# Performance work log

Measured on AMD Instinct MI355X. Metric: run time of the kernel, lower is better.

The kernel has to match this reference:

```python
import jax, jax.numpy as jnp
import numpy as np

HIDDEN = 1024
HEADS = 16
HEAD_DIM = 64
EPS = 0.001  # numerical_stabilizer


def setup_inputs() -> dict:
    key = jax.random.key(0)
    kq, kk, kv, kwq, kwk, kwv = jax.random.split(key, 6)
    B, S = 4, 4096
    shape = (B, S, HIDDEN)
    # glorot_uniform over (hidden, heads*head_dim) fan
    init = jax.nn.initializers.glorot_uniform()
    wshape = (HIDDEN, HEADS, HEAD_DIM)
    return {
        "query": jax.random.normal(kq, shape, jnp.float32),
        "key": jax.random.normal(kk, shape, jnp.float32),
        "value": jax.random.normal(kv, shape, jnp.float32),
        "query_kernel": init(kwq, wshape, jnp.float32),
        "key_kernel": init(kwk, wshape, jnp.float32),
        "value_kernel": init(kwv, wshape, jnp.float32),
    }


def reference(query, key, value, query_kernel, key_kernel, value_kernel):
    # project: [b,s,d] x [d,n,h] -> [b,s,n,h]
    q = jnp.einsum('bsd,dnh->bsnh', query, query_kernel)
    k = jnp.einsum('bsd,dnh->bsnh', key, key_kernel)
    v = jnp.einsum('bsd,dnh->bsnh', value, value_kernel)
    # relu feature map + stabilizer
    q = jax.nn.relu(q) + EPS
    k = jax.nn.relu(k) + EPS
    # kv aggregation: [b,n,h_k,h_v]
    kvs = jnp.einsum('bsnm,bsnd->bnmd', k, v)
    a_v = jnp.einsum('bsnm,bnmd->bsnd', q, kvs)
    ks_sum = jnp.sum(k, axis=1)                 # [b,n,m]
    normalizer = jnp.einsum('bsnm,bnm->bsn', q, ks_sum)
    a_v = a_v / normalizer[..., None]
    B, S, N, H = a_v.shape
    return a_v.reshape(B, S, N * H)
```

## Files before the change

kernel.cpp:

```cpp
#include <hip/hip_runtime.h>
#include <hip/hip_bf16.h>
#include <cstdint>
#include <cstddef>

#define HIDDEN 1024
#define NHEADS 16
#define HD     64
#define BATCH  4
#define SEQ    4096
#define MTOT   (BATCH*SEQ)
#define EPSF   1e-3f

typedef unsigned short u16;
typedef unsigned int   u32;
typedef __bf16 bf16x8 __attribute__((ext_vector_type(8)));
typedef u16    u16x8  __attribute__((ext_vector_type(8)));
typedef float  f32x4  __attribute__((ext_vector_type(4)));
typedef u32    u32x4  __attribute__((ext_vector_type(4)));

__device__ inline u16 f2bf(float a) {
    __bf16 h = (__bf16)a;
    return __builtin_bit_cast(u16, h);
}
__device__ inline u32 pack2bf(float a, float b) {
    return (u32)f2bf(a) | ((u32)f2bf(b) << 16);
}
__device__ inline float bf2f(u16 x) {
    return __builtin_bit_cast(float, (u32)x << 16);
}
__device__ inline f32x4 mfma16(bf16x8 a, bf16x8 b, f32x4 c) {
    return __builtin_amdgcn_mfma_f32_16x16x32_bf16(a, b, c, 0, 0, 0);
}
__device__ inline void gl_lds16(const void* g, void* l) {
    __builtin_amdgcn_global_load_lds(
        (const __attribute__((address_space(1))) void*)g,
        (__attribute__((address_space(3))) void*)l,
        16, 0, 0);
}

__global__ __launch_bounds__(256) void prep_kernel(
    const float* __restrict__ W0, const float* __restrict__ W1,
    const float* __restrict__ W2, u16* __restrict__ Wt,
    float* __restrict__ zero_base)
{
    const int t = threadIdx.x;
    if (blockIdx.z == 3) {
        const int base = (blockIdx.y * 16 + blockIdx.x) * 256 + t;
        const int total = 64*64*64 + 64*64;
        for (int idx = base; idx < total; idx += 65536) zero_base[idx] = 0.f;
        return;
    }
    const int z = blockIdx.z;
    const float* __restrict__ W = (z == 0) ? W0 : ((z == 1) ? W1 : W2);
    u16* __restrict__ Wz = Wt + (size_t)z * HIDDEN * HIDDEN;
    const int d0 = blockIdx.y * 64, c0 = blockIdx.x * 64;
    __shared__ u16 T[64 * 72];
    {
        const int r = t & 63, p = t >> 6;
        const float* src = W + (size_t)(d0 + r) * HIDDEN + c0 + p * 16;
        f32x4 x0 = *(const f32x4*)src,       x1 = *(const f32x4*)(src + 4);
        f32x4 x2 = *(const f32x4*)(src + 8), x3 = *(const f32x4*)(src + 12);
        u32x4 y0 = { pack2bf(x0[0],x0[1]), pack2bf(x0[2],x0[3]),
                     pack2bf(x1[0],x1[1]), pack2bf(x1[2],x1[3]) };
        u32x4 y1 = { pack2bf(x2[0],x2[1]), pack2bf(x2[2],x2[3]),
                     pack2bf(x3[0],x3[1]), pack2bf(x3[2],x3[3]) };
        *(u32x4*)((char*)T + (size_t)(r * 72 + p * 16) * 2)     = y0;
        *(u32x4*)((char*)T + (size_t)(r * 72 + p * 16 + 8) * 2) = y1;
    }
    __syncthreads();
    {
        const int c = t & 63, p = t >> 6;
        u16 vals[16];
        #pragma unroll
        for (int i = 0; i < 16; ++i) vals[i] = T[(p * 16 + i) * 72 + c];
        u16* dst = Wz + (size_t)(c0 + c) * HIDDEN + d0 + p * 16;
        *(u16x8*)dst       = *(const u16x8*)&vals[0];
        *(u16x8*)(dst + 8) = *(const u16x8*)&vals[8];
    }
}

__global__ __launch_bounds__(256) void conv_kernel(
    const float* __restrict__ X0, const float* __restrict__ X1,
    const float* __restrict__ X2, u16* __restrict__ D0,
    u16* __restrict__ D1, u16* __restrict__ D2)
{
    const int z = blockIdx.y;
    const float* __restrict__ X = (z == 0) ? X0 : ((z == 1) ? X1 : X2);
    u16* __restrict__ D = (z == 0) ? D0 : ((z == 1) ? D1 : D2);
    const int ngrp = MTOT * HIDDEN / 8;
    for (int i = blockIdx.x * 256 + threadIdx.x; i < ngrp; i += 262144) {
        const size_t off = (size_t)i * 8;
        f32x4 a = *(const f32x4*)(X + off);
        f32x4 b = *(const f32x4*)(X + off + 4);
        u32x4 p = { pack2bf(a[0],a[1]), pack2bf(a[2],a[3]),
                    pack2bf(b[0],b[1]), pack2bf(b[2],b[3]) };
        *(u32x4*)(D + off) = p;
    }
}

__global__ __launch_bounds__(256) void gemm_proj(
    const u16* __restrict__ Xb, const u16* __restrict__ W,
    u16* __restrict__ Pz, const int doact)
{
    const int lin = blockIdx.y * 8 + blockIdx.x;
    const int swz = (lin & 7) * 128 + (lin >> 3);
    const int m0 = (swz >> 3) * 128;
    const int n0 = (swz & 7) * 128;

    __shared__ u16 As[128 * 64];
    __shared__ u16 Bs[128 * 64];

    const int t = threadIdx.x, lane = t & 63, wid = t >> 6;
    const int wr = (wid >> 1) * 64, wc = (wid & 1) * 64;
    const int l15 = lane & 15, l4 = lane >> 4;
    const int srow = lane >> 3;
    const int schunk = (lane & 7) ^ srow;

    f32x4 acc[4][4];
    #pragma unroll
    for (int i = 0; i < 4; ++i)
        #pragma unroll
        for (int j = 0; j < 4; ++j) acc[i][j] = f32x4{0.f, 0.f, 0.f, 0.f};

    for (int kt = 0; kt < HIDDEN / 64; ++kt) {
        const int k0 = kt * 64;
        __syncthreads();
        #pragma unroll
        for (int g = 0; g < 4; ++g) {
            const int rbase = wid * 32 + g * 8;
            const int r = rbase + srow;
            gl_lds16(Xb + (size_t)(m0 + r) * HIDDEN + k0 + schunk * 8,
                     &As[rbase * 64]);
            gl_lds16(W + (size_t)(n0 + r) * HIDDEN + k0 + schunk * 8,
                     &Bs[rbase * 64]);
        }
        __syncthreads();
        #pragma unroll
        for (int ks = 0; ks < 2; ++ks) {
            bf16x8 af[4], bfr[4];
            #pragma unroll
            for (int mi = 0; mi < 4; ++mi) {
                const int r = wr + mi * 16 + l15;
                const int c = (ks * 4 + l4) ^ (r & 7);
                af[mi] = *(const bf16x8*)((const char*)As + (size_t)r * 128 + c * 16);
            }
            #pragma unroll
            for (int ni = 0; ni < 4; ++ni) {
                const int r = wc + ni * 16 + l15;
                const int c = (ks * 4 + l4) ^ (r & 7);
                bfr[ni] = *(const bf16x8*)((const char*)Bs + (size_t)r * 128 + c * 16);
            }
            #pragma unroll
            for (int mi = 0; mi < 4; ++mi)
                #pragma unroll
                for (int ni = 0; ni < 4; ++ni)
                    acc[mi][ni] = mfma16(af[mi], bfr[ni], acc[mi][ni]);
        }
    }
    #pragma unroll
    for (int mi = 0; mi < 4; ++mi) {
        #pragma unroll
        for (int ni = 0; ni < 4; ++ni) {
            const int mrow = m0 + wr + mi * 16 + l4 * 4;
            const int ncol = n0 + wc + ni * 16 + l15;
            #pragma unroll
            for (int r = 0; r < 4; ++r) {
                float v = acc[mi][ni][r];
                if (doact) v = fmaxf(v, 0.f) + EPSF;
                Pz[(size_t)(mrow + r) * HIDDEN + ncol] = f2bf(v);
            }
        }
    }
}

__global__ __launch_bounds__(256) void kvs_kernel(
    const u16* __restrict__ Kp, const u16* __restrict__ Vp,
    float* __restrict__ kvsT, float* __restrict__ ks_sum)
{
    const int bn = blockIdx.x, sc = blockIdx.y;
    const int b = bn >> 4, n = bn & 15;
    __shared__ float Ks[64 * 64];
    __shared__ float Vs[64 * 64];
    const int t = threadIdx.x;
    const int tm = t & 15, td = t >> 4;
    float acc[4][4] = {};
    float ksa[4] = {0.f, 0.f, 0.f, 0.f};
    const size_t rowbase = ((size_t)b * SEQ + (size_t)sc * 256) * HIDDEN + n * 64;

    for (int st = 0; st < 4; ++st) {
        __syncthreads();
        #pragma unroll
        for (int i = 0; i < 2; ++i) {
            const int j = i * 256 + t;
            const int r = j >> 3, c = j & 7;
            const size_t off = rowbase + (size_t)(st * 64 + r) * HIDDEN + c * 8;
            u16x8 kk = *(const u16x8*)(Kp + off);
            u16x8 vv = *(const u16x8*)(Vp + off);
            f32x4 ka{bf2f(kk[0]), bf2f(kk[1]), bf2f(kk[2]), bf2f(kk[3])};
            f32x4 kb{bf2f(kk[4]), bf2f(kk[5]), bf2f(kk[6]), bf2f(kk[7])};
            f32x4 va{bf2f(vv[0]), bf2f(vv[1]), bf2f(vv[2]), bf2f(vv[3])};
            f32x4 vb{bf2f(vv[4]), bf2f(vv[5]), bf2f(vv[6]), bf2f(vv[7])};
            *(f32x4*)&Ks[r * 64 + c * 8]     = ka;
            *(f32x4*)&Ks[r * 64 + c * 8 + 4] = kb;
            *(f32x4*)&Vs[r * 64 + c * 8]     = va;
            *(f32x4*)&Vs[r * 64 + c * 8 + 4] = vb;
        }
        __syncthreads();
        for (int s = 0; s < 64; ++s) {
            const f32x4 kk = *(const f32x4*)&Ks[s * 64 + tm * 4];
            const f32x4 vv = *(const f32x4*)&Vs[s * 64 + td * 4];
            #pragma unroll
            for (int i = 0; i < 4; ++i) {
                ksa[i] += kk[i];
                #pragma unroll
                for (int j = 0; j < 4; ++j) acc[i][j] += kk[i] * vv[j];
            }
        }
    }
    float* kt_bn = kvsT + (size_t)bn * 64 * 64;
    #pragma unroll
    for (int j = 0; j < 4; ++j)
        #pragma unroll
        for (int i = 0; i < 4; ++i)
            atomicAdd(&kt_bn[(td * 4 + j) * 64 + tm * 4 + i], acc[i][j]);
    if (td == 0) {
        #pragma unroll
        for (int i = 0; i < 4; ++i)
            atomicAdd(&ks_sum[bn * 64 + tm * 4 + i], ksa[i]);
    }
}

__global__ __launch_bounds__(256) void out_kernel(
    const u16* __restrict__ Qp, const float* __restrict__ kvsT,
    const float* __restrict__ ks_sum, float* __restrict__ out)
{
    const int bn = blockIdx.x, sc = blockIdx.y;
    const int b = bn >> 4, n = bn & 15;
    __shared__ u16 Aq[256 * 64];
    __shared__ u16 Bk[64 * 64];
    __shared__ float ksl[64];
    __shared__ float nrm[256];
    const int t = threadIdx.x, lane = t & 63, wid = t >> 6;
    const int l15 = lane & 15, l4 = lane >> 4;
    const size_t qbase = ((size_t)b * SEQ + (size_t)sc * 256) * HIDDEN + n * 64;

    #pragma unroll
    for (int i = 0; i < 8; ++i) {
        const int j = i * 256 + t;
        const int r = j >> 3, c = j & 7;
        u16x8 q8 = *(const u16x8*)(Qp + qbase + (size_t)r * HIDDEN + c * 8);
        *(u16x8*)((char*)Aq + (size_t)r * 128 + ((c ^ (r & 7)) * 16)) = q8;
    }
    {
        const int d = t & 63, p = t >> 6;
        const float* src = kvsT + ((size_t)bn * 64 + d) * 64 + p * 16;
        f32x4 x0 = *(const f32x4*)src,        x1 = *(const f32x4*)(src + 4);
        f32x4 x2 = *(const f32x4*)(src + 8),  x3 = *(const f32x4*)(src + 12);
        u32x4 y0 = { pack2bf(x0[0],x0[1]), pack2bf(x0[2],x0[3]),
                     pack2bf(x1[0],x1[1]), pack2bf(x1[2],x1[3]) };
        u32x4 y1 = { pack2bf(x2[0],x2[1]), pack2bf(x2[2],x2[3]),
                     pack2bf(x3[0],x3[1]), pack2bf(x3[2],x3[3]) };
        *(u32x4*)((char*)Bk + (size_t)d * 128 + (((p * 2)     ^ (d & 7)) * 16)) = y0;
        *(u32x4*)((char*)Bk + (size_t)d * 128 + (((p * 2 + 1) ^ (d & 7)) * 16)) = y1;
    }
    if (t < 16) ((f32x4*)ksl)[t] = ((const f32x4*)(ks_sum + bn * 64))[t];
    __syncthreads();
    {
        float s = 0.f;
        #pragma unroll
        for (int c = 0; c < 8; ++c) {
            u16x8 q8 = *(const u16x8*)((const char*)Aq + (size_t)t * 128 + ((c ^ (t & 7)) * 16));
            #pragma unroll
            for (int e = 0; e < 8; ++e) s += bf2f(q8[e]) * ksl[c * 8 + e];
        }
        nrm[t] = s;
    }
    __syncthreads();
    f32x4 acc[4][4];
    #pragma unroll
    for (int i = 0; i < 4; ++i)
        #pragma unroll
        for (int j = 0; j < 4; ++j) acc[i][j] = f32x4{0.f, 0.f, 0.f, 0.f};
    #pragma unroll
    for (int ks = 0; ks < 2; ++ks) {
        bf16x8 af[4], bfr[4];
        #pragma unroll
        for (int mi = 0; mi < 4; ++mi) {
            const int r = wid * 64 + mi * 16 + l15;
            const int c = (ks * 4 + l4) ^ (r & 7);
            af[mi] = *(const bf16x8*)((const char*)Aq + (size_t)r * 128 + c * 16);
        }
        #pragma unroll
        for (int ni = 0; ni < 4; ++ni) {
            const int rd = ni * 16 + l15;
            const int c = (ks * 4 + l4) ^ (rd & 7);
            bfr[ni] = *(const bf16x8*)((const char*)Bk + (size_t)rd * 128 + c * 16);
        }
        #pragma unroll
        for (int mi = 0; mi < 4; ++mi)
            #pragma unroll
            for (int ni = 0; ni < 4; ++ni)
                acc[mi][ni] = mfma16(af[mi], bfr[ni], acc[mi][ni]);
    }
    const size_t obase = (size_t)b * SEQ + (size_t)sc * 256;
    #pragma unroll
    for (int mi = 0; mi < 4; ++mi) {
        const int s0l = wid * 64 + mi * 16 + l4 * 4;
        const float rn0 = 1.f / nrm[s0l],     rn1 = 1.f / nrm[s0l + 1];
        const float rn2 = 1.f / nrm[s0l + 2], rn3 = 1.f / nrm[s0l + 3];
        #pragma unroll
        for (int ni = 0; ni < 4; ++ni) {
            const int d = ni * 16 + l15;
            float* op = out + (obase + s0l) * (size_t)HIDDEN + n * 64 + d;
            op[0 * HIDDEN] = acc[mi][ni][0] * rn0;
            op[1 * HIDDEN] = acc[mi][ni][1] * rn1;
            op[2 * HIDDEN] = acc[mi][ni][2] * rn2;
            op[3 * HIDDEN] = acc[mi][ni][3] * rn3;
        }
    }
}

extern "C" void kernel_launch(void* const* d_in, const int* in_sizes, int n_in,
                              void* d_out, int out_size, void* d_ws, size_t ws_size,
                              hipStream_t stream)
{
    const float* Xq = (const float*)d_in[0];
    const float* Xk = (const float*)d_in[1];
    const float* Xv = (const float*)d_in[2];
    const float* Wq = (const float*)d_in[3];
    const float* Wk = (const float*)d_in[4];
    const float* Wv = (const float*)d_in[5];
    float* out = (float*)d_out;

    char* w = (char*)d_ws;
    u16*   Wt    = (u16*)w;
    u16*   slotA = (u16*)(w + 6291456);
    u16*   slotB = (u16*)(w + 6291456 + 1 * 33554432);
    u16*   slotC = (u16*)(w + 6291456 + 2 * 33554432);
    u16*   slotD = (u16*)(w + 6291456 + 3 * 33554432);
    float* kvsT  = (float*)(w + 6291456 + 4 * 33554432);
    float* ks    = (float*)(w + 6291456 + 4 * 33554432 + 1048576);

    prep_kernel<<<dim3(16, 16, 4), 256, 0, stream>>>(Wq, Wk, Wv, Wt, kvsT);
    conv_kernel<<<dim3(1024, 3), 256, 0, stream>>>(Xq, Xk, Xv, slotA, slotB, slotC);
    gemm_proj<<<dim3(8, 128), 256, 0, stream>>>(slotA, Wt,                 slotD, 1);
    gemm_proj<<<dim3(8, 128), 256, 0, stream>>>(slotB, Wt + 1048576,       slotA, 1);
    gemm_proj<<<dim3(8, 128), 256, 0, stream>>>(slotC, Wt + 2 * 1048576,   slotB, 0);
    kvs_kernel<<<dim3(64, 16), 256, 0, stream>>>(slotA, slotB, kvsT, ks);
    out_kernel<<<dim3(64, 16), 256, 0, stream>>>(slotD, kvsT, ks, out);
}
```

Baseline: 476.2 us.

## Fuse fp32-to-bf16 input conversion into projection GEMM and batch three projections

Removes the separate conversion kernel. The projection GEMM now reads fp32 activations directly, prefetching the next k-tile into registers and packing to bf16 into swizzled LDS. The three projection GEMMs are merged into one launch over blockIdx.z. This avoids writing and re-reading a bf16 copy of the 3x64MB inputs and drops two kernel launches. In exchange each tile reads twice the bytes, the A operand goes through registers instead of async global-to-LDS loads, and register pressure rises.

Result: faster. 465.2 us (-2.3%).

```diff
diff --git a/kernel.cpp b/kernel.cpp
--- a/kernel.cpp
+++ b/kernel.cpp
@@ -79,29 +79,17 @@
     }
 }
 
-__global__ __launch_bounds__(256) void conv_kernel(
+__global__ __launch_bounds__(256) void gemm_proj(
     const float* __restrict__ X0, const float* __restrict__ X1,
-    const float* __restrict__ X2, u16* __restrict__ D0,
-    u16* __restrict__ D1, u16* __restrict__ D2)
-{
-    const int z = blockIdx.y;
+    const float* __restrict__ X2, const u16* __restrict__ Wt,
+    u16* __restrict__ P)
+{
+    const int z = blockIdx.z;
     const float* __restrict__ X = (z == 0) ? X0 : ((z == 1) ? X1 : X2);
-    u16* __restrict__ D = (z == 0) ? D0 : ((z == 1) ? D1 : D2);
-    const int ngrp = MTOT * HIDDEN / 8;
-    for (int i = blockIdx.x * 256 + threadIdx.x; i < ngrp; i += 262144) {
-        const size_t off = (size_t)i * 8;
-        f32x4 a = *(const f32x4*)(X + off);
-        f32x4 b = *(const f32x4*)(X + off + 4);
-        u32x4 p = { pack2bf(a[0],a[1]), pack2bf(a[2],a[3]),
-                    pack2bf(b[0],b[1]), pack2bf(b[2],b[3]) };
-        *(u32x4*)(D + off) = p;
-    }
-}
-
-__global__ __launch_bounds__(256) void gemm_proj(
-    const u16* __restrict__ Xb, const u16* __restrict__ W,
-    u16* __restrict__ Pz, const int doact)
-{
+    const u16* __restrict__ W = Wt + (size_t)z * HIDDEN * HIDDEN;
+    u16* __restrict__ Pz = P + (size_t)z * ((size_t)MTOT * HIDDEN);
+    const int doact = (z < 2);
+
     const int lin = blockIdx.y * 8 + blockIdx.x;
     const int swz = (lin & 7) * 128 + (lin >> 3);
     const int m0 = (swz >> 3) * 128;
@@ -113,26 +101,49 @@
     const int t = threadIdx.x, lane = t & 63, wid = t >> 6;
     const int wr = (wid >> 1) * 64, wc = (wid & 1) * 64;
     const int l15 = lane & 15, l4 = lane >> 4;
-    const int srow = lane >> 3;
-    const int schunk = (lane & 7) ^ srow;
+    const int arow = t >> 3, acol = t & 7;
+    const int brow = lane >> 3;
+    const int bchunk = (lane & 7) ^ brow;
 
     f32x4 acc[4][4];
     #pragma unroll
     for (int i = 0; i < 4; ++i)
         #pragma unroll
         for (int j = 0; j < 4; ++j) acc[i][j] = f32x4{0.f, 0.f, 0.f, 0.f};
+
+    f32x4 a0[4], a1[4];
+    #pragma unroll
+    for (int i = 0; i < 4; ++i) {
+        const float* ap = X + (size_t)(m0 + arow + 32 * i) * HIDDEN + acol * 8;
+        a0[i] = *(const f32x4*)ap;
+        a1[i] = *(const f32x4*)(ap + 4);
+    }
 
     for (int kt = 0; kt < HIDDEN / 64; ++kt) {
         const int k0 = kt * 64;
         __syncthreads();
         #pragma unroll
+        for (int i = 0; i < 4; ++i) {
+            const int r = arow + 32 * i;
+            const int cd = acol ^ (r & 7);
+            u32x4 apk = { pack2bf(a0[i][0], a0[i][1]), pack2bf(a0[i][2], a0[i][3]),
+                          pack2bf(a1[i][0], a1[i][1]), pack2bf(a1[i][2], a1[i][3]) };
+            *(u32x4*)((char*)As + (size_t)r * 128 + cd * 16) = apk;
+        }
+        #pragma unroll
         for (int g = 0; g < 4; ++g) {
             const int rbase = wid * 32 + g * 8;
-            const int r = rbase + srow;
-            gl_lds16(Xb + (size_t)(m0 + r) * HIDDEN + k0 + schunk * 8,
-                     &As[rbase * 64]);
-            gl_lds16(W + (size_t)(n0 + r) * HIDDEN + k0 + schunk * 8,
+            gl_lds16(W + (size_t)(n0 + rbase + brow) * HIDDEN + k0 + bchunk * 8,
                      &Bs[rbase * 64]);
+        }
+        if (kt + 1 < HIDDEN / 64) {
+            #pragma unroll
+            for (int i = 0; i < 4; ++i) {
+                const float* ap = X + (size_t)(m0 + arow + 32 * i) * HIDDEN
+                                    + (k0 + 64) + acol * 8;
+                a0[i] = *(const f32x4*)ap;
+                a1[i] = *(const f32x4*)(ap + 4);
+            }
         }
         __syncthreads();
         #pragma unroll
@@ -333,19 +344,16 @@
     float* out = (float*)d_out;
 
     char* w = (char*)d_ws;
-    u16*   Wt    = (u16*)w;
-    u16*   slotA = (u16*)(w + 6291456);
-    u16*   slotB = (u16*)(w + 6291456 + 1 * 33554432);
-    u16*   slotC = (u16*)(w + 6291456 + 2 * 33554432);
-    u16*   slotD = (u16*)(w + 6291456 + 3 * 33554432);
-    float* kvsT  = (float*)(w + 6291456 + 4 * 33554432);
-    float* ks    = (float*)(w + 6291456 + 4 * 33554432 + 1048576);
+    u16*   Wt   = (u16*)w;
+    u16*   P    = (u16*)(w + 6291456);
+    u16*   Pq   = P;
+    u16*   Pk   = P + (size_t)MTOT * HIDDEN;
+    u16*   Pv   = P + 2 * (size_t)MTOT * HIDDEN;
+    float* kvsT = (float*)(w + 6291456 + 3 * 33554432);
+    float* ks   = (float*)(w + 6291456 + 3 * 33554432 + 1048576);
 
     prep_kernel<<<dim3(16, 16, 4), 256, 0, stream>>>(Wq, Wk, Wv, Wt, kvsT);
-    conv_kernel<<<dim3(1024, 3), 256, 0, stream>>>(Xq, Xk, Xv, slotA, slotB, slotC);
-    gemm_proj<<<dim3(8, 128), 256, 0, stream>>>(slotA, Wt,                 slotD, 1);
-    gemm_proj<<<dim3(8, 128), 256, 0, stream>>>(slotB, Wt + 1048576,       slotA, 1);
-    gemm_proj<<<dim3(8, 128), 256, 0, stream>>>(slotC, Wt + 2 * 1048576,   slotB, 0);
-    kvs_kernel<<<dim3(64, 16), 256, 0, stream>>>(slotA, slotB, kvsT, ks);
-    out_kernel<<<dim3(64, 16), 256, 0, stream>>>(slotD, kvsT, ks, out);
-}
+    gemm_proj<<<dim3(8, 128, 3), 256, 0, stream>>>(Xq, Xk, Xv, Wt, P);
+    kvs_kernel<<<dim3(64, 16), 256, 0, stream>>>(Pk, Pv, kvsT, ks);
+    out_kernel<<<dim3(64, 16), 256, 0, stream>>>(Pq, kvsT, ks, out);
+}
```

## Double-buffer GEMM LDS tiles, widen conv loads, halve kvs grid

Applied to the files above, without the earlier changes.

The projection GEMM now uses two LDS buffers, so the async global-to-LDS load of the next K tile is issued while MFMAs run on the current one, with one barrier per iteration instead of two. The conversion kernel is unrolled to a fixed four iterations of 16 elements per thread, giving more memory requests in flight. The kvs kernel processes 512 sequence rows per block over half as many blocks. Costs are doubled LDS use in the GEMM, which may reduce occupancy, and less parallelism in kvs.

Result: faster. 463.0 us (-2.8%).

```diff
diff --git a/kernel.cpp b/kernel.cpp
--- a/kernel.cpp
+++ b/kernel.cpp
@@ -87,14 +87,20 @@
     const int z = blockIdx.y;
     const float* __restrict__ X = (z == 0) ? X0 : ((z == 1) ? X1 : X2);
     u16* __restrict__ D = (z == 0) ? D0 : ((z == 1) ? D1 : D2);
-    const int ngrp = MTOT * HIDDEN / 8;
-    for (int i = blockIdx.x * 256 + threadIdx.x; i < ngrp; i += 262144) {
-        const size_t off = (size_t)i * 8;
-        f32x4 a = *(const f32x4*)(X + off);
-        f32x4 b = *(const f32x4*)(X + off + 4);
-        u32x4 p = { pack2bf(a[0],a[1]), pack2bf(a[2],a[3]),
-                    pack2bf(b[0],b[1]), pack2bf(b[2],b[3]) };
-        *(u32x4*)(D + off) = p;
+    const int tid = blockIdx.x * 256 + threadIdx.x;
+    #pragma unroll
+    for (int it = 0; it < 4; ++it) {
+        const size_t off = ((size_t)(it * 262144 + tid)) * 16;
+        f32x4 x0 = *(const f32x4*)(X + off);
+        f32x4 x1 = *(const f32x4*)(X + off + 4);
+        f32x4 x2 = *(const f32x4*)(X + off + 8);
+        f32x4 x3 = *(const f32x4*)(X + off + 12);
+        u32x4 p0 = { pack2bf(x0[0],x0[1]), pack2bf(x0[2],x0[3]),
+                     pack2bf(x1[0],x1[1]), pack2bf(x1[2],x1[3]) };
+        u32x4 p1 = { pack2bf(x2[0],x2[1]), pack2bf(x2[2],x2[3]),
+                     pack2bf(x3[0],x3[1]), pack2bf(x3[2],x3[3]) };
+        *(u32x4*)(D + off)     = p0;
+        *(u32x4*)(D + off + 8) = p1;
     }
 }
 
@@ -107,14 +113,14 @@
     const int m0 = (swz >> 3) * 128;
     const int n0 = (swz & 7) * 128;
 
-    __shared__ u16 As[128 * 64];
-    __shared__ u16 Bs[128 * 64];
+    __shared__ u16 As[2][128 * 64];
+    __shared__ u16 Bs[2][128 * 64];
 
     const int t = threadIdx.x, lane = t & 63, wid = t >> 6;
     const int wr = (wid >> 1) * 64, wc = (wid & 1) * 64;
     const int l15 = lane & 15, l4 = lane >> 4;
-    const int srow = lane >> 3;
-    const int schunk = (lane & 7) ^ srow;
+    const int brow = lane >> 3;
+    const int bchunk = (lane & 7) ^ brow;
 
     f32x4 acc[4][4];
     #pragma unroll
@@ -122,19 +128,26 @@
         #pragma unroll
         for (int j = 0; j < 4; ++j) acc[i][j] = f32x4{0.f, 0.f, 0.f, 0.f};
 
-    for (int kt = 0; kt < HIDDEN / 64; ++kt) {
-        const int k0 = kt * 64;
-        __syncthreads();
-        #pragma unroll
-        for (int g = 0; g < 4; ++g) {
-            const int rbase = wid * 32 + g * 8;
-            const int r = rbase + srow;
-            gl_lds16(Xb + (size_t)(m0 + r) * HIDDEN + k0 + schunk * 8,
-                     &As[rbase * 64]);
-            gl_lds16(W + (size_t)(n0 + r) * HIDDEN + k0 + schunk * 8,
-                     &Bs[rbase * 64]);
-        }
-        __syncthreads();
+#define STAGE(BUF, KT)                                                       \
+    {                                                                        \
+        _Pragma("unroll")                                                    \
+        for (int g = 0; g < 4; ++g) {                                        \
+            const int rbase = wid * 32 + g * 8;                              \
+            gl_lds16(Xb + (size_t)(m0 + rbase + brow) * HIDDEN               \
+                        + (KT) * 64 + bchunk * 8,                            \
+                     &As[BUF][rbase * 64]);                                  \
+            gl_lds16(W + (size_t)(n0 + rbase + brow) * HIDDEN                \
+                       + (KT) * 64 + bchunk * 8,                             \
+                     &Bs[BUF][rbase * 64]);                                  \
+        }                                                                    \
+    }
+
+    STAGE(0, 0);
+    __syncthreads();
+
+    for (int kt = 0; kt < 16; ++kt) {
+        const int cur = kt & 1;
+        if (kt + 1 < 16) STAGE(cur ^ 1, kt + 1);
         #pragma unroll
         for (int ks = 0; ks < 2; ++ks) {
             bf16x8 af[4], bfr[4];
@@ -142,13 +155,13 @@
             for (int mi = 0; mi < 4; ++mi) {
                 const int r = wr + mi * 16 + l15;
                 const int c = (ks * 4 + l4) ^ (r & 7);
-                af[mi] = *(const bf16x8*)((const char*)As + (size_t)r * 128 + c * 16);
+                af[mi] = *(const bf16x8*)((const char*)As[cur] + (size_t)r * 128 + c * 16);
             }
             #pragma unroll
             for (int ni = 0; ni < 4; ++ni) {
                 const int r = wc + ni * 16 + l15;
                 const int c = (ks * 4 + l4) ^ (r & 7);
-                bfr[ni] = *(const bf16x8*)((const char*)Bs + (size_t)r * 128 + c * 16);
+                bfr[ni] = *(const bf16x8*)((const char*)Bs[cur] + (size_t)r * 128 + c * 16);
             }
             #pragma unroll
             for (int mi = 0; mi < 4; ++mi)
@@ -156,7 +169,10 @@
                 for (int ni = 0; ni < 4; ++ni)
                     acc[mi][ni] = mfma16(af[mi], bfr[ni], acc[mi][ni]);
         }
-    }
+        __syncthreads();
+    }
+#undef STAGE
+
     #pragma unroll
     for (int mi = 0; mi < 4; ++mi) {
         #pragma unroll
@@ -185,9 +201,9 @@
     const int tm = t & 15, td = t >> 4;
     float acc[4][4] = {};
     float ksa[4] = {0.f, 0.f, 0.f, 0.f};
-    const size_t rowbase = ((size_t)b * SEQ + (size_t)sc * 256) * HIDDEN + n * 64;
-
-    for (int st = 0; st < 4; ++st) {
+    const size_t rowbase = ((size_t)b * SEQ + (size_t)sc * 512) * HIDDEN + n * 64;
+
+    for (int st = 0; st < 8; ++st) {
         __syncthreads();
         #pragma unroll
         for (int i = 0; i < 2; ++i) {
@@ -343,9 +359,9 @@
 
     prep_kernel<<<dim3(16, 16, 4), 256, 0, stream>>>(Wq, Wk, Wv, Wt, kvsT);
     conv_kernel<<<dim3(1024, 3), 256, 0, stream>>>(Xq, Xk, Xv, slotA, slotB, slotC);
-    gemm_proj<<<dim3(8, 128), 256, 0, stream>>>(slotA, Wt,                 slotD, 1);
-    gemm_proj<<<dim3(8, 128), 256, 0, stream>>>(slotB, Wt + 1048576,       slotA, 1);
-    gemm_proj<<<dim3(8, 128), 256, 0, stream>>>(slotC, Wt + 2 * 1048576,   slotB, 0);
-    kvs_kernel<<<dim3(64, 16), 256, 0, stream>>>(slotA, slotB, kvsT, ks);
+    gemm_proj<<<dim3(8, 128), 256, 0, stream>>>(slotA, Wt,               slotD, 1);
+    gemm_proj<<<dim3(8, 128), 256, 0, stream>>>(slotB, Wt + 1048576,     slotA, 1);
+    gemm_proj<<<dim3(8, 128), 256, 0, stream>>>(slotC, Wt + 2 * 1048576, slotB, 0);
+    kvs_kernel<<<dim3(64, 8), 256, 0, stream>>>(slotA, slotB, kvsT, ks);
     out_kernel<<<dim3(64, 16), 256, 0, stream>>>(slotD, kvsT, ks, out);
 }
```
